# Performance work log

Measured on AMD Instinct MI355X. Metric: run time of the kernel, lower is better.

## Reference

```python
import jax, jax.numpy as jnp
import numpy as np

B, T, DSEQ = 4096, 128, 128
DMEAN, DPRIOR = 256, 256
H, DOUT = 256, 128
NEXP, SCALE = 4, 0.1
NUM_EDGES = max(1, int(B * B * 0.05))  # static top-k size


def setup_inputs() -> dict:
    key = jax.random.key(0)
    ks = jax.random.split(key, 20)
    def n(k, shape):
        return jax.random.normal(k, shape, dtype=jnp.float32) * 0.02
    z = lambda *s: jnp.zeros(s, jnp.float32)
    return {
        "input_seq": jax.random.normal(ks[0], (B, T, DSEQ), dtype=jnp.float32),
        "mean_embedding": jax.random.normal(ks[1], (B, DMEAN), dtype=jnp.float32),
        "prior_target": jax.random.normal(ks[2], (B, DPRIOR), dtype=jnp.float32),
        "gru_Wih0": n(ks[3], (3 * H, DSEQ)), "gru_Whh0": n(ks[4], (3 * H, H)),
        "gru_bih0": z(3 * H), "gru_bhh0": z(3 * H),
        "gru_Wih1": n(ks[5], (3 * H, H)), "gru_Whh1": n(ks[6], (3 * H, H)),
        "gru_bih1": z(3 * H), "gru_bhh1": z(3 * H),
        "fc_mean_W": n(ks[7], (H, DMEAN)), "fc_mean_b": z(H),
        "gru_fc_W": n(ks[8], (DOUT, 2 * H)), "gru_fc_b": z(DOUT),
        "gcn1_W": n(ks[9], (H, DPRIOR)), "gcn1_b": z(H),
        "gcn2_W": n(ks[10], (H, H)), "gcn2_b": z(H),
        "prior_fc_W": n(ks[11], (DOUT, H)), "prior_fc_b": z(DOUT),
        "expert_W": n(ks[12], (NEXP, DOUT, DOUT)),
        "attn1_W": n(ks[13], (DOUT, 2 * DOUT)), "attn1_b": z(DOUT),
        "attn2_W": n(ks[14], (NEXP, DOUT)), "attn2_b": z(NEXP),
    }


def _gru_layer(x, Wih, Whh, bih, bhh):
    # x: [B,T,D]; PyTorch GRU cell equations
    h_dim = Whh.shape[1]
    def step(h, xt):
        gi = xt @ Wih.T + bih            # [B,3H]
        gh = h @ Whh.T + bhh
        i_r, i_z, i_n = jnp.split(gi, 3, axis=-1)
        h_r, h_z, h_n = jnp.split(gh, 3, axis=-1)
        r = jax.nn.sigmoid(i_r + h_r)
        zg = jax.nn.sigmoid(i_z + h_z)
        ng = jnp.tanh(i_n + r * h_n)
        h_new = (1.0 - zg) * ng + zg * h
        return h_new, h_new
    h0 = jnp.zeros((x.shape[0], h_dim), x.dtype)
    _, ys = jax.lax.scan(step, h0, jnp.swapaxes(x, 0, 1))
    return jnp.swapaxes(ys, 0, 1)


def _gcn(x, W, b, src, dst, n_nodes):
    # PyG GCNConv: add self-loops, sym-normalized mean aggregation
    loop = jnp.arange(n_nodes)
    s = jnp.concatenate([src, loop])
    d = jnp.concatenate([dst, loop])
    deg = jax.ops.segment_sum(jnp.ones(s.shape, x.dtype), d, num_segments=n_nodes)
    dinv = jnp.where(deg > 0, jax.lax.rsqrt(deg), 0.0)
    norm = dinv[s] * dinv[d]                  # [E]
    xw = x @ W.T                              # [N,H]
    out = jax.ops.segment_sum(xw[s] * norm[:, None], d, num_segments=n_nodes)
    return out + b


def reference(input_seq, mean_embedding, prior_target,
              gru_Wih0, gru_Whh0, gru_bih0, gru_bhh0,
              gru_Wih1, gru_Whh1, gru_bih1, gru_bhh1,
              fc_mean_W, fc_mean_b, gru_fc_W, gru_fc_b,
              gcn1_W, gcn1_b, gcn2_W, gcn2_b,
              prior_fc_W, prior_fc_b, expert_W,
              attn1_W, attn1_b, attn2_W, attn2_b):
    # --- GRU branch ---
    h1 = _gru_layer(input_seq, gru_Wih0, gru_Whh0, gru_bih0, gru_bhh0)
    h2 = _gru_layer(h1, gru_Wih1, gru_Whh1, gru_bih1, gru_bhh1)
    last_hidden = h2[:, -1, :]
    mean_feat = jax.nn.relu(mean_embedding @ fc_mean_W.T + fc_mean_b)
    gru_feat = jnp.concatenate([last_hidden, mean_feat], axis=1)
    gru_out_proj = gru_feat @ gru_fc_W.T + gru_fc_b          # [B,DOUT]
    # --- dynamic graph build via similarity top-k ---
    sim = prior_target @ prior_target.T                      # [B,B]
    diag = jnp.arange(B)
    sim = sim.at[diag, diag].set(0.0)
    _, topk_idx = jax.lax.top_k(sim.reshape(-1), NUM_EDGES)
    row = topk_idx // B
    col = topk_idx % B
    src = jnp.concatenate([row, col])   # symmetrized edge list
    dst = jnp.concatenate([col, row])
    # --- GCN branch ---
    ph = jax.nn.relu(_gcn(prior_target, gcn1_W, gcn1_b, src, dst, B))
    ph = jax.nn.relu(_gcn(ph, gcn2_W, gcn2_b, src, dst, B))
    prior_out = ph @ prior_fc_W.T + prior_fc_b               # [B,DOUT]
    # --- attention expert gate fusion ---
    base = 0.5 * gru_out_proj + 0.5 * prior_out
    diff = gru_out_proj - prior_out
    expert_res = jnp.einsum('eod,bd->beo', expert_W, diff)   # [B,NEXP,DOUT]
    fused = jnp.concatenate([gru_out_proj, prior_out], axis=-1)
    hatt = jnp.tanh(fused @ attn1_W.T + attn1_b)
    w = jax.nn.softmax(hatt @ attn2_W.T + attn2_b, axis=-1)  # [B,NEXP]
    delta = jnp.einsum('be,beo->bo', w, expert_res)
    pred = base + SCALE * delta
    return pred, gru_out_proj, prior_out
```

## Files before the change

kernel.cpp:

```cpp
#include <hip/hip_runtime.h>
#include <hip/hip_bf16.h>

#define BB    4096
#define TT    128
#define DSEQ_ 128
#define HH    256
#define DOUT_ 128
#define NEXP_ 4
static const long NUM_EDGES_ = 838860;

typedef _Float16 f16;
typedef _Float16 f16x8 __attribute__((ext_vector_type(8)));
typedef float    f32x4 __attribute__((ext_vector_type(4)));

__global__ void pack_weights_kernel(const float* __restrict__ Wih,
                                    const float* __restrict__ Whh,
                                    f16* __restrict__ Wp, int Din)
{
    const int K = Din + HH;
    const int total = 1024 * K;
    for (int idx = blockIdx.x * 256 + threadIdx.x; idx < total; idx += gridDim.x * 256) {
        int n = idx / K, k = idx % K;
        int u = n >> 2, g = n & 3;
        float v = 0.f;
        if (k < Din) {
            if (g == 0)      v = Wih[(long)u * Din + k];
            else if (g == 1) v = Wih[(long)(256 + u) * Din + k];
            else if (g == 2) v = Wih[(long)(512 + u) * Din + k];
        } else {
            int kh = k - Din;
            if (g == 0)      v = Whh[(long)u * HH + kh];
            else if (g == 1) v = Whh[(long)(256 + u) * HH + kh];
            else if (g == 3) v = Whh[(long)(512 + u) * HH + kh];
        }
        Wp[idx] = (f16)v;
    }
}

__global__ void pack_bias_kernel(const float* __restrict__ bih,
                                 const float* __restrict__ bhh,
                                 float* __restrict__ bias)
{
    int n = blockIdx.x * 256 + threadIdx.x;
    if (n >= 1024) return;
    int u = n >> 2, g = n & 3;
    float v;
    if (g == 0)      v = bih[u] + bhh[u];
    else if (g == 1) v = bih[256 + u] + bhh[256 + u];
    else if (g == 2) v = bih[512 + u];
    else             v = bhh[512 + u];
    bias[n] = v;
}

__global__ __launch_bounds__(256) void gru_superstep(
    const f16* __restrict__ Wp0, const float* __restrict__ bias0,
    const float* __restrict__ xseq,
    const f16* __restrict__ h1_in, f16* __restrict__ h1_out, int t0,
    const f16* __restrict__ Wp1, const float* __restrict__ bias1,
    const f16* __restrict__ h1_x,
    const f16* __restrict__ h2_in, f16* __restrict__ h2_out, int t1)
{
    const int layer = blockIdx.z;
    if (layer == 0 && t0 >= TT) return;
    if (layer == 1 && t1 < 0) return;

    const f16* Wp; const float* bias;
    const f16* ax16 = nullptr;
    const f16* hprev; f16* hout;
    int xc, K; long xstride = 0, xoff = 0;
    if (layer == 0) {
        Wp = Wp0; bias = bias0; xc = DSEQ_; K = DSEQ_ + HH;
        xstride = (long)TT * DSEQ_; xoff = (long)t0 * DSEQ_;
        hprev = h1_in; hout = h1_out;
    } else {
        Wp = Wp1; bias = bias1; ax16 = h1_x; xc = HH; K = HH + HH;
        hprev = h2_in; hout = h2_out;
    }

    __shared__ f16 As[128 * 32];
    __shared__ f16 Bs[128 * 32];

    const int tid  = threadIdx.x;
    const int srow = tid >> 1;
    const int sc0  = (tid & 1) * 16;
    const long m0  = (long)blockIdx.x * 128;
    const int  n0  = blockIdx.y * 128;

    const int wave = tid >> 6, lane = tid & 63;
    const int wm = wave >> 1, wn = wave & 1;
    const int quad = lane >> 4, l15 = lane & 15;

    f32x4 acc[4][4];
#pragma unroll
    for (int i = 0; i < 4; i++)
#pragma unroll
        for (int j = 0; j < 4; j++) acc[i][j] = (f32x4){0.f, 0.f, 0.f, 0.f};

    const int nchunks = K >> 5;
    for (int kc = 0; kc < nchunks; kc++) {
        const int k0 = kc << 5;
        __syncthreads();
        {
            int kg = k0 + sc0;
            f16* dst = &As[srow * 32 + sc0];
            if (kg < xc) {
                if (layer == 0) {
                    const float* p = xseq + (m0 + srow) * xstride + xoff + kg;
#pragma unroll
                    for (int j = 0; j < 16; j += 4) {
                        float4 v = *(const float4*)(p + j);
                        dst[j] = (f16)v.x; dst[j + 1] = (f16)v.y;
                        dst[j + 2] = (f16)v.z; dst[j + 3] = (f16)v.w;
                    }
                } else {
                    const f16* p = ax16 + (m0 + srow) * HH + kg;
                    *(float4*)dst       = *(const float4*)p;
                    *(float4*)(dst + 8) = *(const float4*)(p + 8);
                }
            } else {
                const f16* p = hprev + (m0 + srow) * HH + (kg - xc);
                *(float4*)dst       = *(const float4*)p;
                *(float4*)(dst + 8) = *(const float4*)(p + 8);
            }
        }
        {
            const f16* p = Wp + (long)(n0 + srow) * K + k0 + sc0;
            f16* dst = &Bs[srow * 32 + sc0];
            *(float4*)dst       = *(const float4*)p;
            *(float4*)(dst + 8) = *(const float4*)(p + 8);
        }
        __syncthreads();

        f16x8 af[4], bf[4];
#pragma unroll
        for (int i = 0; i < 4; i++)
            af[i] = *(const f16x8*)&As[(wm * 64 + i * 16 + l15) * 32 + quad * 8];
#pragma unroll
        for (int i = 0; i < 4; i++)
            bf[i] = *(const f16x8*)&Bs[(wn * 64 + i * 16 + l15) * 32 + quad * 8];
#pragma unroll
        for (int mi = 0; mi < 4; mi++)
#pragma unroll
            for (int ni = 0; ni < 4; ni++)
                acc[mi][ni] = __builtin_amdgcn_mfma_f32_16x16x32_f16(af[mi], bf[ni], acc[mi][ni], 0, 0, 0);
    }

    const long mbase = m0 + wm * 64;
    const int  nbase = n0 + wn * 64;
#pragma unroll
    for (int mi = 0; mi < 4; mi++) {
#pragma unroll
        for (int ni = 0; ni < 4; ni++) {
            const int ncol = nbase + ni * 16 + l15;
            const float bn = bias[ncol];
#pragma unroll
            for (int reg = 0; reg < 4; reg++) {
                float v = acc[mi][ni][reg] + bn;
                const int gb = lane & ~3;
                float g0 = __shfl(v, gb + 0, 64);
                float g1 = __shfl(v, gb + 1, 64);
                float g2 = __shfl(v, gb + 2, 64);
                float g3 = __shfl(v, gb + 3, 64);
                if ((lane & 3) == 0) {
                    const long mrow = mbase + mi * 16 + quad * 4 + reg;
                    const int u = ncol >> 2;
                    float hp = (float)hprev[mrow * HH + u];
                    float r = 1.f / (1.f + __expf(-g0));
                    float z = 1.f / (1.f + __expf(-g1));
                    float ng = 1.f - 2.f / (__expf(2.f * (g2 + r * g3)) + 1.f);
                    float hn = (1.f - z) * ng + z * hp;
                    hout[mrow * HH + u] = (f16)hn;
                }
            }
        }
    }
}

__global__ __launch_bounds__(256) void gemm_bt_kernel(
    const float* __restrict__ A, const float* __restrict__ Bm, float* __restrict__ C,
    int M, int N, int K, const float* __restrict__ bias,
    const float* __restrict__ rscale, int act)
{
    __shared__ float As[16][65];
    __shared__ float Bs[16][65];
    const int tid = threadIdx.x;
    const long m0 = (long)blockIdx.x * 64;
    const int  n0 = blockIdx.y * 64;
    const int ty = tid >> 4, tx = tid & 15;
    const int mA = tid >> 2, kq = (tid & 3) * 4;
    float c[4][4] = {};
    for (int k0 = 0; k0 < K; k0 += 16) {
        __syncthreads();
        float4 va = *(const float4*)&A[(m0 + mA) * K + k0 + kq];
        As[kq + 0][mA] = va.x; As[kq + 1][mA] = va.y; As[kq + 2][mA] = va.z; As[kq + 3][mA] = va.w;
        float4 vb = *(const float4*)&Bm[(long)(n0 + mA) * K + k0 + kq];
        Bs[kq + 0][mA] = vb.x; Bs[kq + 1][mA] = vb.y; Bs[kq + 2][mA] = vb.z; Bs[kq + 3][mA] = vb.w;
        __syncthreads();
#pragma unroll
        for (int k = 0; k < 16; k++) {
            float a4[4], b4[4];
#pragma unroll
            for (int j = 0; j < 4; j++) { a4[j] = As[k][ty * 4 + j]; b4[j] = Bs[k][tx * 4 + j]; }
#pragma unroll
            for (int i = 0; i < 4; i++)
#pragma unroll
                for (int j = 0; j < 4; j++) c[i][j] = fmaf(a4[i], b4[j], c[i][j]);
        }
    }
#pragma unroll
    for (int i = 0; i < 4; i++) {
        const long m = m0 + ty * 4 + i;
        const float rs = rscale ? rscale[m] : 1.f;
#pragma unroll
        for (int j = 0; j < 4; j++) {
            const int n = n0 + tx * 4 + j;
            float v = c[i][j] * rs;
            if (bias) v += bias[n];
            if (act == 1) v = fmaxf(v, 0.f);
            else if (act == 2) v = tanhf(v);
            C[m * N + n] = v;
        }
    }
}

__global__ void zero_diag_kernel(float* __restrict__ sim)
{
    int i = blockIdx.x * 256 + threadIdx.x;
    if (i < BB) sim[(long)i * BB + i] = 0.f;
}

__device__ inline unsigned keyOf(float f)
{
    unsigned u = __float_as_uint(f);
    return (u & 0x80000000u) ? ~u : (u | 0x80000000u);
}

__global__ void hist_kernel(const float* __restrict__ sim, unsigned* __restrict__ hist,
                            const unsigned* __restrict__ state, int pass)
{
    __shared__ unsigned h[4096];
    for (int i = threadIdx.x; i < 4096; i += 256) h[i] = 0;
    __syncthreads();
    unsigned pfx1 = 0, pfx2 = 0;
    if (pass == 1) pfx1 = state[0];
    if (pass == 2) pfx2 = state[2];
    const long ntot = (long)BB * BB;
    for (long i = (long)blockIdx.x * 256 + threadIdx.x; i < ntot; i += (long)gridDim.x * 256) {
        unsigned key = keyOf(sim[i]);
        if (pass == 0) atomicAdd(&h[key >> 20], 1u);
        else if (pass == 1) { if ((key >> 20) == pfx1) atomicAdd(&h[(key >> 8) & 0xFFFu], 1u); }
        else               { if ((key >> 8) == pfx2)  atomicAdd(&h[key & 0xFFu], 1u); }
    }
    __syncthreads();
    const int nb = (pass == 2) ? 256 : 4096;
    for (int i = threadIdx.x; i < nb; i += 256)
        if (h[i]) atomicAdd(&hist[i], h[i]);
}

__global__ void scan_hist_kernel(const unsigned* __restrict__ hist, unsigned* __restrict__ state, int pass)
{
    if (threadIdx.x != 0 || blockIdx.x != 0) return;
    long k = (pass == 0) ? NUM_EDGES_ : (long)state[2 * pass - 1];
    const int nb = (pass == 2) ? 256 : 4096;
    long cum = 0; int b = nb - 1;
    for (; b >= 0; b--) { cum += hist[b]; if (cum >= k) break; }
    long kk = k - (cum - hist[b]);
    if (pass == 0) { state[0] = (unsigned)b; state[1] = (unsigned)kk; }
    else if (pass == 1) { state[2] = (state[0] << 12) | (unsigned)b; state[3] = (unsigned)kk; }
    else {
        unsigned key = (state[2] << 8) | (unsigned)b;
        state[4] = key;
        unsigned u = (key & 0x80000000u) ? (key ^ 0x80000000u) : ~key;
        state[5] = u;
    }
}

__global__ void degree_kernel(const float* __restrict__ sim, const unsigned* __restrict__ state,
                              float* __restrict__ dinv)
{
    const float thr = __uint_as_float(state[5]);
    const int d = blockIdx.x;
    const float* row = sim + (long)d * BB;
    int cnt = 0;
    for (int s = threadIdx.x; s < BB; s += 256) cnt += (row[s] >= thr) ? 1 : 0;
    for (int o = 32; o; o >>= 1) cnt += __shfl_down(cnt, o, 64);
    __shared__ int sh[4];
    if ((threadIdx.x & 63) == 0) sh[threadIdx.x >> 6] = cnt;
    __syncthreads();
    if (threadIdx.x == 0) {
        int tot = sh[0] + sh[1] + sh[2] + sh[3];
        dinv[d] = rsqrtf((float)(2 * tot + 1));
    }
}

__global__ __launch_bounds__(256) void gcn_agg_kernel(
    const float* __restrict__ sim, const float* __restrict__ xws,
    const float* __restrict__ dinv, const float* __restrict__ bias,
    const unsigned* __restrict__ state, float* __restrict__ out)
{
    const float thr = __uint_as_float(state[5]);
    __shared__ float As[16][65];
    __shared__ float Bs[16][65];
    const int tid = threadIdx.x;
    const long m0 = (long)blockIdx.x * 64;
    const int  n0 = blockIdx.y * 64;
    const int ty = tid >> 4, tx = tid & 15;
    const int mA = tid >> 2, kq = (tid & 3) * 4;
    const int kB = tid >> 4, nq = (tid & 15) * 4;
    float c[4][4] = {};
    for (int s0 = 0; s0 < BB; s0 += 16) {
        __syncthreads();
        float4 va = *(const float4*)&sim[(m0 + mA) * (long)BB + s0 + kq];
        As[kq + 0][mA] = (va.x >= thr) ? 1.f : 0.f;
        As[kq + 1][mA] = (va.y >= thr) ? 1.f : 0.f;
        As[kq + 2][mA] = (va.z >= thr) ? 1.f : 0.f;
        As[kq + 3][mA] = (va.w >= thr) ? 1.f : 0.f;
        float4 vb = *(const float4*)&xws[(long)(s0 + kB) * HH + n0 + nq];
        Bs[kB][nq + 0] = vb.x; Bs[kB][nq + 1] = vb.y; Bs[kB][nq + 2] = vb.z; Bs[kB][nq + 3] = vb.w;
        __syncthreads();
#pragma unroll
        for (int k = 0; k < 16; k++) {
            float a4[4], b4[4];
#pragma unroll
            for (int j = 0; j < 4; j++) { a4[j] = As[k][ty * 4 + j]; b4[j] = Bs[k][tx * 4 + j]; }
#pragma unroll
            for (int i = 0; i < 4; i++)
#pragma unroll
                for (int j = 0; j < 4; j++) c[i][j] = fmaf(a4[i], b4[j], c[i][j]);
        }
    }
#pragma unroll
    for (int i = 0; i < 4; i++) {
        const long m = m0 + ty * 4 + i;
        const float dv = dinv[m];
#pragma unroll
        for (int j = 0; j < 4; j++) {
            const int n = n0 + tx * 4 + j;
            float v = dv * (2.f * c[i][j] + xws[m * HH + n]) + bias[n];
            out[m * HH + n] = fmaxf(v, 0.f);
        }
    }
}

__global__ void build_gru_feat_kernel(const f16* __restrict__ h2, const float* __restrict__ mf,
                                      float* __restrict__ gf)
{
    long i = (long)blockIdx.x * 256 + threadIdx.x;
    if (i >= (long)BB * 512) return;
    long b = i >> 9; int c = (int)(i & 511);
    gf[i] = (c < 256) ? (float)h2[b * HH + c] : mf[b * HH + (c - 256)];
}

__global__ void build_fused_diff_kernel(const float* __restrict__ g, const float* __restrict__ p,
                                        float* __restrict__ fused, float* __restrict__ diff)
{
    long i = (long)blockIdx.x * 256 + threadIdx.x;
    if (i >= (long)BB * 256) return;
    long b = i >> 8; int c = (int)(i & 255);
    if (c < 128) {
        float gv = g[b * 128 + c], pv = p[b * 128 + c];
        fused[i] = gv;
        diff[b * 128 + c] = gv - pv;
    } else {
        fused[i] = p[b * 128 + (c - 128)];
    }
}

__global__ __launch_bounds__(128) void final_kernel(
    const float* __restrict__ hatt, const float* __restrict__ attn2W, const float* __restrict__ attn2b,
    const float* __restrict__ er, const float* __restrict__ g, const float* __restrict__ p,
    float* __restrict__ pred)
{
    const int b = blockIdx.x;
    __shared__ float w4[4];
    __shared__ float hrow[128];
    const int tid = threadIdx.x;
    hrow[tid] = hatt[(long)b * 128 + tid];
    __syncthreads();
    if (tid < 4) {
        float s = attn2b[tid];
        for (int d = 0; d < 128; d++) s += hrow[d] * attn2W[tid * 128 + d];
        w4[tid] = s;
    }
    __syncthreads();
    if (tid == 0) {
        float mx = fmaxf(fmaxf(w4[0], w4[1]), fmaxf(w4[2], w4[3]));
        float e0 = __expf(w4[0] - mx), e1 = __expf(w4[1] - mx);
        float e2 = __expf(w4[2] - mx), e3 = __expf(w4[3] - mx);
        float inv = 1.f / (e0 + e1 + e2 + e3);
        w4[0] = e0 * inv; w4[1] = e1 * inv; w4[2] = e2 * inv; w4[3] = e3 * inv;
    }
    __syncthreads();
    const long off = (long)b * 128 + tid;
    const long E = (long)BB * DOUT_;
    float base = 0.5f * g[off] + 0.5f * p[off];
    float delta = w4[0] * er[off] + w4[1] * er[off + E] + w4[2] * er[off + 2 * E] + w4[3] * er[off + 3 * E];
    pred[off] = base + 0.1f * delta;
}

extern "C" void kernel_launch(void* const* d_in, const int* in_sizes, int n_in,
                              void* d_out, int out_size, void* d_ws, size_t ws_size,
                              hipStream_t stream)
{
    const float* input_seq  = (const float*)d_in[0];
    const float* mean_emb   = (const float*)d_in[1];
    const float* prior      = (const float*)d_in[2];
    const float* Wih0       = (const float*)d_in[3];
    const float* Whh0       = (const float*)d_in[4];
    const float* bih0       = (const float*)d_in[5];
    const float* bhh0       = (const float*)d_in[6];
    const float* Wih1       = (const float*)d_in[7];
    const float* Whh1       = (const float*)d_in[8];
    const float* bih1       = (const float*)d_in[9];
    const float* bhh1       = (const float*)d_in[10];
    const float* fc_mean_W  = (const float*)d_in[11];
    const float* fc_mean_b  = (const float*)d_in[12];
    const float* gru_fc_W   = (const float*)d_in[13];
    const float* gru_fc_b   = (const float*)d_in[14];
    const float* gcn1_W     = (const float*)d_in[15];
    const float* gcn1_b     = (const float*)d_in[16];
    const float* gcn2_W     = (const float*)d_in[17];
    const float* gcn2_b     = (const float*)d_in[18];
    const float* prior_fc_W = (const float*)d_in[19];
    const float* prior_fc_b = (const float*)d_in[20];
    const float* expert_W   = (const float*)d_in[21];
    const float* attn1_W    = (const float*)d_in[22];
    const float* attn1_b    = (const float*)d_in[23];
    const float* attn2_W    = (const float*)d_in[24];
    const float* attn2_b    = (const float*)d_in[25];

    float* out_pred = (float*)d_out;
    float* out_g    = out_pred + (long)BB * DOUT_;
    float* out_p    = out_g + (long)BB * DOUT_;

    char* base = (char*)d_ws;
    size_t off = 0;
    auto alloc = [&](size_t bytes) -> char* {
        char* p = base + off;
        off = (off + bytes + 255) & ~(size_t)255;
        return p;
    };
    f16*   wp0    = (f16*)alloc((size_t)1024 * 384 * 2);
    f16*   wp1    = (f16*)alloc((size_t)1024 * 512 * 2);
    float* bias0  = (float*)alloc(1024 * 4);
    float* bias1  = (float*)alloc(1024 * 4);
    f16*   h1b[2]; h1b[0] = (f16*)alloc((size_t)BB * HH * 2); h1b[1] = (f16*)alloc((size_t)BB * HH * 2);
    f16*   h2b[2]; h2b[0] = (f16*)alloc((size_t)BB * HH * 2); h2b[1] = (f16*)alloc((size_t)BB * HH * 2);
    float* sim    = (float*)alloc((size_t)BB * BB * 4);
    unsigned* hist  = (unsigned*)alloc(4096 * 4);
    unsigned* state = (unsigned*)alloc(256);
    float* dinv   = (float*)alloc(BB * 4);
    float* mf     = (float*)alloc((size_t)BB * HH * 4);
    float* gf     = (float*)alloc((size_t)BB * 2 * HH * 4);
    float* xws1   = (float*)alloc((size_t)BB * HH * 4);
    float* ph1    = (float*)alloc((size_t)BB * HH * 4);
    float* xws2   = (float*)alloc((size_t)BB * HH * 4);
    float* ph2    = (float*)alloc((size_t)BB * HH * 4);
    float* diffb  = (float*)alloc((size_t)BB * DOUT_ * 4);
    float* fusedb = (float*)alloc((size_t)BB * 2 * DOUT_ * 4);
    float* hatt   = (float*)alloc((size_t)BB * DOUT_ * 4);
    float* er     = (float*)alloc((size_t)NEXP_ * BB * DOUT_ * 4);
    if (off > ws_size) return;

    pack_weights_kernel<<<1536, 256, 0, stream>>>(Wih0, Whh0, wp0, DSEQ_);
    pack_weights_kernel<<<2048, 256, 0, stream>>>(Wih1, Whh1, wp1, HH);
    pack_bias_kernel<<<4, 256, 0, stream>>>(bih0, bhh0, bias0);
    pack_bias_kernel<<<4, 256, 0, stream>>>(bih1, bhh1, bias1);
    hipMemsetAsync(h1b[0], 0, (size_t)BB * HH * 2, stream);
    hipMemsetAsync(h1b[1], 0, (size_t)BB * HH * 2, stream);
    hipMemsetAsync(h2b[0], 0, (size_t)BB * HH * 2, stream);
    hipMemsetAsync(h2b[1], 0, (size_t)BB * HH * 2, stream);

    for (int tau = 0; tau <= TT; tau++) {
        gru_superstep<<<dim3(32, 8, 2), 256, 0, stream>>>(
            wp0, bias0, input_seq, h1b[tau & 1], h1b[(tau + 1) & 1], tau,
            wp1, bias1, h1b[tau & 1], h2b[tau & 1], h2b[(tau + 1) & 1], tau - 1);
    }
    const f16* h2fin = h2b[(TT + 1) & 1];

    gemm_bt_kernel<<<dim3(64, 4), 256, 0, stream>>>(mean_emb, fc_mean_W, mf, BB, HH, 256, fc_mean_b, nullptr, 1);
    build_gru_feat_kernel<<<(BB * 512) / 256, 256, 0, stream>>>(h2fin, mf, gf);
    gemm_bt_kernel<<<dim3(64, 2), 256, 0, stream>>>(gf, gru_fc_W, out_g, BB, DOUT_, 512, gru_fc_b, nullptr, 0);

    gemm_bt_kernel<<<dim3(64, 64), 256, 0, stream>>>(prior, prior, sim, BB, BB, 256, nullptr, nullptr, 0);
    zero_diag_kernel<<<16, 256, 0, stream>>>(sim);
    for (int pass = 0; pass < 3; pass++) {
        hipMemsetAsync(hist, 0, 4096 * 4, stream);
        hist_kernel<<<1024, 256, 0, stream>>>(sim, hist, state, pass);
        scan_hist_kernel<<<1, 64, 0, stream>>>(hist, state, pass);
    }
    degree_kernel<<<BB, 256, 0, stream>>>(sim, state, dinv);

    gemm_bt_kernel<<<dim3(64, 4), 256, 0, stream>>>(prior, gcn1_W, xws1, BB, HH, 256, nullptr, dinv, 0);
    gcn_agg_kernel<<<dim3(64, 4), 256, 0, stream>>>(sim, xws1, dinv, gcn1_b, state, ph1);
    gemm_bt_kernel<<<dim3(64, 4), 256, 0, stream>>>(ph1, gcn2_W, xws2, BB, HH, 256, nullptr, dinv, 0);
    gcn_agg_kernel<<<dim3(64, 4), 256, 0, stream>>>(sim, xws2, dinv, gcn2_b, state, ph2);
    gemm_bt_kernel<<<dim3(64, 2), 256, 0, stream>>>(ph2, prior_fc_W, out_p, BB, DOUT_, 256, prior_fc_b, nullptr, 0);

    build_fused_diff_kernel<<<(BB * 256) / 256, 256, 0, stream>>>(out_g, out_p, fusedb, diffb);
    for (int e = 0; e < NEXP_; e++)
        gemm_bt_kernel<<<dim3(64, 2), 256, 0, stream>>>(diffb, expert_W + (long)e * DOUT_ * DOUT_,
                                                        er + (long)e * BB * DOUT_, BB, DOUT_, DOUT_,
                                                        nullptr, nullptr, 0);
    gemm_bt_kernel<<<dim3(64, 2), 256, 0, stream>>>(fusedb, attn1_W, hatt, BB, DOUT_, 256, attn1_b, nullptr, 2);
    final_kernel<<<BB, 128, 0, stream>>>(hatt, attn2_W, attn2_b, er, out_g, out_p, out_pred);
}
```

Baseline: 6.207 ms.

## Move similarity and GCN aggregation GEMMs to fp16 MFMA with async LDS loads

The GRU superstep now loads its operands through global_load_lds direct-to-LDS transfers via a shared mm_async helper. The similarity matrix is computed with MFMA using a split hi/lo fp16 packing (three products) to keep near-fp32 accuracy, and the diagonal is zeroed inside the same kernel. The two GCN aggregation GEMMs over the 4096x4096 thresholded adjacency now run on fp16 MFMA with a split-K of four, then a combine kernel reduces the partials. Workspace buffers are aliased into one shared region to save memory. The fp16 rounding of the aggregated features and the hi/lo approximation of the similarity could change top-k tie-breaking and accuracy.

```diff
diff --git a/kernel.cpp b/kernel.cpp
--- a/kernel.cpp
+++ b/kernel.cpp
@@ -12,6 +12,10 @@
 typedef _Float16 f16;
 typedef _Float16 f16x8 __attribute__((ext_vector_type(8)));
 typedef float    f32x4 __attribute__((ext_vector_type(4)));
+
+#define GLL(gp, lp) __builtin_amdgcn_global_load_lds( \
+    (const __attribute__((address_space(1))) void*)(gp), \
+    (__attribute__((address_space(3))) void*)(lp), 16, 0, 0)
 
 __global__ void pack_weights_kernel(const float* __restrict__ Wih,
                                     const float* __restrict__ Whh,
@@ -52,6 +56,41 @@
     bias[n] = v;
 }
 
+__device__ __forceinline__ void mm_async(
+    f32x4 (&acc)[4][4], f16* __restrict__ As, f16* __restrict__ Bs,
+    const f16* __restrict__ Ag, long lda, const f16* __restrict__ Bg, long ldb,
+    int kChunks, int wave, int lane)
+{
+    const int r0 = wave * 32 + (lane >> 2);
+    const int ce = (lane & 3) * 8;
+    const int wm = wave >> 1, wn = wave & 1;
+    const int quad = lane >> 4, l15 = lane & 15;
+    const f16* ag0 = Ag + (long)r0 * lda + ce;
+    const f16* ag1 = ag0 + 16 * lda;
+    const f16* bg0 = Bg + (long)r0 * ldb + ce;
+    const f16* bg1 = bg0 + 16 * ldb;
+    f16* asw = As + wave * 1024;
+    f16* bsw = Bs + wave * 1024;
+    for (int kc = 0; kc < kChunks; kc++) {
+        __syncthreads();
+        GLL(ag0, asw); GLL(ag1, asw + 512);
+        GLL(bg0, bsw); GLL(bg1, bsw + 512);
+        ag0 += 32; ag1 += 32; bg0 += 32; bg1 += 32;
+        __syncthreads();
+        f16x8 af[4], bf[4];
+#pragma unroll
+        for (int i = 0; i < 4; i++) {
+            af[i] = *(const f16x8*)&As[(wm * 64 + i * 16 + l15) * 32 + quad * 8];
+            bf[i] = *(const f16x8*)&Bs[(wn * 64 + i * 16 + l15) * 32 + quad * 8];
+        }
+#pragma unroll
+        for (int mi = 0; mi < 4; mi++)
+#pragma unroll
+            for (int ni = 0; ni < 4; ni++)
+                acc[mi][ni] = __builtin_amdgcn_mfma_f32_16x16x32_f16(af[mi], bf[ni], acc[mi][ni], 0, 0, 0);
+    }
+}
+
 __global__ __launch_bounds__(256) void gru_superstep(
     const f16* __restrict__ Wp0, const float* __restrict__ bias0,
     const float* __restrict__ xseq,
@@ -64,31 +103,14 @@
     if (layer == 0 && t0 >= TT) return;
     if (layer == 1 && t1 < 0) return;
 
-    const f16* Wp; const float* bias;
-    const f16* ax16 = nullptr;
-    const f16* hprev; f16* hout;
-    int xc, K; long xstride = 0, xoff = 0;
-    if (layer == 0) {
-        Wp = Wp0; bias = bias0; xc = DSEQ_; K = DSEQ_ + HH;
-        xstride = (long)TT * DSEQ_; xoff = (long)t0 * DSEQ_;
-        hprev = h1_in; hout = h1_out;
-    } else {
-        Wp = Wp1; bias = bias1; ax16 = h1_x; xc = HH; K = HH + HH;
-        hprev = h2_in; hout = h2_out;
-    }
-
-    __shared__ f16 As[128 * 32];
-    __shared__ f16 Bs[128 * 32];
-
-    const int tid  = threadIdx.x;
-    const int srow = tid >> 1;
-    const int sc0  = (tid & 1) * 16;
-    const long m0  = (long)blockIdx.x * 128;
-    const int  n0  = blockIdx.y * 128;
-
+    __shared__ f16 As[4096];
+    __shared__ f16 Bs[4096];
+    const int tid = threadIdx.x;
     const int wave = tid >> 6, lane = tid & 63;
     const int wm = wave >> 1, wn = wave & 1;
     const int quad = lane >> 4, l15 = lane & 15;
+    const long m0 = (long)blockIdx.x * 128;
+    const int  n0 = blockIdx.y * 128;
 
     f32x4 acc[4][4];
 #pragma unroll
@@ -96,53 +118,50 @@
 #pragma unroll
         for (int j = 0; j < 4; j++) acc[i][j] = (f32x4){0.f, 0.f, 0.f, 0.f};
 
-    const int nchunks = K >> 5;
-    for (int kc = 0; kc < nchunks; kc++) {
-        const int k0 = kc << 5;
-        __syncthreads();
-        {
-            int kg = k0 + sc0;
-            f16* dst = &As[srow * 32 + sc0];
-            if (kg < xc) {
-                if (layer == 0) {
-                    const float* p = xseq + (m0 + srow) * xstride + xoff + kg;
-#pragma unroll
-                    for (int j = 0; j < 16; j += 4) {
-                        float4 v = *(const float4*)(p + j);
-                        dst[j] = (f16)v.x; dst[j + 1] = (f16)v.y;
-                        dst[j + 2] = (f16)v.z; dst[j + 3] = (f16)v.w;
-                    }
-                } else {
-                    const f16* p = ax16 + (m0 + srow) * HH + kg;
-                    *(float4*)dst       = *(const float4*)p;
-                    *(float4*)(dst + 8) = *(const float4*)(p + 8);
-                }
-            } else {
-                const f16* p = hprev + (m0 + srow) * HH + (kg - xc);
-                *(float4*)dst       = *(const float4*)p;
-                *(float4*)(dst + 8) = *(const float4*)(p + 8);
+    const f16* hprev; f16* hout; const float* bias;
+    if (layer == 0) {
+        hprev = h1_in; hout = h1_out; bias = bias0;
+        const int arow = tid >> 1, ac0 = (tid & 1) * 16;
+        const float* ap = xseq + (m0 + arow) * ((long)TT * DSEQ_) + (long)t0 * DSEQ_ + ac0;
+        const int r0 = wave * 32 + (lane >> 2);
+        const int ce = (lane & 3) * 8;
+        const f16* bg0 = Wp0 + (long)(n0 + r0) * 384 + ce;
+        const f16* bg1 = bg0 + 16 * 384;
+        f16* bsw = Bs + wave * 1024;
+        for (int kc = 0; kc < 4; kc++) {
+            float4 v0 = *(const float4*)(ap + 0);
+            float4 v1 = *(const float4*)(ap + 4);
+            float4 v2 = *(const float4*)(ap + 8);
+            float4 v3 = *(const float4*)(ap + 12);
+            ap += 32;
+            __syncthreads();
+            f16x8 w0, w1;
+            w0[0] = (f16)v0.x; w0[1] = (f16)v0.y; w0[2] = (f16)v0.z; w0[3] = (f16)v0.w;
+            w0[4] = (f16)v1.x; w0[5] = (f16)v1.y; w0[6] = (f16)v1.z; w0[7] = (f16)v1.w;
+            w1[0] = (f16)v2.x; w1[1] = (f16)v2.y; w1[2] = (f16)v2.z; w1[3] = (f16)v2.w;
+            w1[4] = (f16)v3.x; w1[5] = (f16)v3.y; w1[6] = (f16)v3.z; w1[7] = (f16)v3.w;
+            *(f16x8*)&As[arow * 32 + ac0]     = w0;
+            *(f16x8*)&As[arow * 32 + ac0 + 8] = w1;
+            GLL(bg0, bsw); GLL(bg1, bsw + 512);
+            bg0 += 32; bg1 += 32;
+            __syncthreads();
+            f16x8 af[4], bf[4];
+#pragma unroll
+            for (int i = 0; i < 4; i++) {
+                af[i] = *(const f16x8*)&As[(wm * 64 + i * 16 + l15) * 32 + quad * 8];
+                bf[i] = *(const f16x8*)&Bs[(wn * 64 + i * 16 + l15) * 32 + quad * 8];
             }
+#pragma unroll
+            for (int mi = 0; mi < 4; mi++)
+#pragma unroll
+                for (int ni = 0; ni < 4; ni++)
+                    acc[mi][ni] = __builtin_amdgcn_mfma_f32_16x16x32_f16(af[mi], bf[ni], acc[mi][ni], 0, 0, 0);
         }
-        {
-            const f16* p = Wp + (long)(n0 + srow) * K + k0 + sc0;
-            f16* dst = &Bs[srow * 32 + sc0];
-            *(float4*)dst       = *(const float4*)p;
-            *(float4*)(dst + 8) = *(const float4*)(p + 8);
-        }
-        __syncthreads();
-
-        f16x8 af[4], bf[4];
-#pragma unroll
-        for (int i = 0; i < 4; i++)
-            af[i] = *(const f16x8*)&As[(wm * 64 + i * 16 + l15) * 32 + quad * 8];
-#pragma unroll
-        for (int i = 0; i < 4; i++)
-            bf[i] = *(const f16x8*)&Bs[(wn * 64 + i * 16 + l15) * 32 + quad * 8];
-#pragma unroll
-        for (int mi = 0; mi < 4; mi++)
-#pragma unroll
-            for (int ni = 0; ni < 4; ni++)
-                acc[mi][ni] = __builtin_amdgcn_mfma_f32_16x16x32_f16(af[mi], bf[ni], acc[mi][ni], 0, 0, 0);
+        mm_async(acc, As, Bs, h1_in + m0 * HH, HH, Wp0 + (long)n0 * 384 + 128, 384, 8, wave, lane);
+    } else {
+        hprev = h2_in; hout = h2_out; bias = bias1;
+        mm_async(acc, As, Bs, h1_x + m0 * HH, HH, Wp1 + (long)n0 * 512, 512, 8, wave, lane);
+        mm_async(acc, As, Bs, h2_in + m0 * HH, HH, Wp1 + (long)n0 * 512 + 256, 512, 8, wave, lane);
     }
 
     const long mbase = m0 + wm * 64;
@@ -176,6 +195,217 @@
     }
 }
 
+__global__ void sim_pack_kernel(const float* __restrict__ prior,
+                                f16* __restrict__ pA, f16* __restrict__ pB)
+{
+    int i = blockIdx.x * 256 + threadIdx.x;
+    if (i >= BB * 256) return;
+    int b = i >> 8, k = i & 255;
+    float v = prior[i];
+    f16 hi = (f16)v;
+    f16 lo = (f16)(v - (float)hi);
+    long r = (long)b * 768;
+    pA[r + k] = hi; pA[r + 256 + k] = hi; pA[r + 512 + k] = lo;
+    pB[r + k] = hi; pB[r + 256 + k] = lo; pB[r + 512 + k] = hi;
+}
+
+__global__ __launch_bounds__(256) void sim_mm_kernel(
+    const f16* __restrict__ pA, const f16* __restrict__ pB, float* __restrict__ sim)
+{
+    __shared__ f16 As[4096];
+    __shared__ f16 Bs[4096];
+    const int tid = threadIdx.x;
+    const int wave = tid >> 6, lane = tid & 63;
+    const int wm = wave >> 1, wn = wave & 1;
+    const int quad = lane >> 4, l15 = lane & 15;
+    const long m0 = (long)blockIdx.x * 128;
+    const int  n0 = blockIdx.y * 128;
+    f32x4 acc[4][4];
+#pragma unroll
+    for (int i = 0; i < 4; i++)
+#pragma unroll
+        for (int j = 0; j < 4; j++) acc[i][j] = (f32x4){0.f, 0.f, 0.f, 0.f};
+    mm_async(acc, As, Bs, pA + m0 * 768, 768, pB + (long)n0 * 768, 768, 24, wave, lane);
+    const long mbase = m0 + wm * 64;
+    const int  nbase = n0 + wn * 64;
+#pragma unroll
+    for (int mi = 0; mi < 4; mi++)
+#pragma unroll
+        for (int ni = 0; ni < 4; ni++)
+#pragma unroll
+            for (int reg = 0; reg < 4; reg++) {
+                long row = mbase + mi * 16 + quad * 4 + reg;
+                int col = nbase + ni * 16 + l15;
+                float v = acc[mi][ni][reg];
+                if (row == (long)col) v = 0.f;
+                sim[row * BB + col] = v;
+            }
+}
+
+__device__ inline unsigned keyOf(float f)
+{
+    unsigned u = __float_as_uint(f);
+    return (u & 0x80000000u) ? ~u : (u | 0x80000000u);
+}
+
+__global__ void hist_kernel(const float* __restrict__ sim, unsigned* __restrict__ hist,
+                            const unsigned* __restrict__ state, int pass)
+{
+    __shared__ unsigned h[4096];
+    for (int i = threadIdx.x; i < 4096; i += 256) h[i] = 0;
+    __syncthreads();
+    unsigned pfx1 = 0, pfx2 = 0;
+    if (pass == 1) pfx1 = state[0];
+    if (pass == 2) pfx2 = state[2];
+    const long ntot = (long)BB * BB;
+    for (long i = (long)blockIdx.x * 256 + threadIdx.x; i < ntot; i += (long)gridDim.x * 256) {
+        unsigned key = keyOf(sim[i]);
+        if (pass == 0) atomicAdd(&h[key >> 20], 1u);
+        else if (pass == 1) { if ((key >> 20) == pfx1) atomicAdd(&h[(key >> 8) & 0xFFFu], 1u); }
+        else               { if ((key >> 8) == pfx2)  atomicAdd(&h[key & 0xFFu], 1u); }
+    }
+    __syncthreads();
+    const int nb = (pass == 2) ? 256 : 4096;
+    for (int i = threadIdx.x; i < nb; i += 256)
+        if (h[i]) atomicAdd(&hist[i], h[i]);
+}
+
+__global__ void scan_hist_kernel(const unsigned* __restrict__ hist,
+                                 unsigned* __restrict__ state, int pass)
+{
+    __shared__ unsigned hl[4096];
+    const int nb = (pass == 2) ? 256 : 4096;
+    for (int i = threadIdx.x; i < nb; i += 256) hl[i] = hist[i];
+    __syncthreads();
+    if (threadIdx.x != 0 || blockIdx.x != 0) return;
+    long k = (pass == 0) ? NUM_EDGES_ : (long)state[2 * pass - 1];
+    long cum = 0; int b = nb - 1;
+    for (; b >= 0; b--) { cum += hl[b]; if (cum >= k) break; }
+    long kk = k - (cum - hl[b]);
+    if (pass == 0) { state[0] = (unsigned)b; state[1] = (unsigned)kk; }
+    else if (pass == 1) { state[2] = (state[0] << 12) | (unsigned)b; state[3] = (unsigned)kk; }
+    else {
+        unsigned key = (state[2] << 8) | (unsigned)b;
+        state[4] = key;
+        unsigned u = (key & 0x80000000u) ? (key ^ 0x80000000u) : ~key;
+        state[5] = u;
+    }
+}
+
+__global__ void degree_kernel(const float* __restrict__ sim, const unsigned* __restrict__ state,
+                              float* __restrict__ dinv)
+{
+    const float thr = __uint_as_float(state[5]);
+    const int d = blockIdx.x;
+    const float* row = sim + (long)d * BB;
+    int cnt = 0;
+    for (int s = threadIdx.x; s < BB; s += 256) cnt += (row[s] >= thr) ? 1 : 0;
+    for (int o = 32; o; o >>= 1) cnt += __shfl_down(cnt, o, 64);
+    __shared__ int sh[4];
+    if ((threadIdx.x & 63) == 0) sh[threadIdx.x >> 6] = cnt;
+    __syncthreads();
+    if (threadIdx.x == 0) {
+        int tot = sh[0] + sh[1] + sh[2] + sh[3];
+        dinv[d] = rsqrtf((float)(2 * tot + 1));
+    }
+}
+
+__global__ void txp_kernel(const float* __restrict__ xws, f16* __restrict__ bT)
+{
+    int i = blockIdx.x * 256 + threadIdx.x;
+    if (i >= BB * 256) return;
+    int n = i >> 12, m = i & 4095;
+    bT[(long)n * BB + m] = (f16)xws[(long)m * 256 + n];
+}
+
+__global__ __launch_bounds__(256) void gcn_mm_kernel(
+    const float* __restrict__ sim, const f16* __restrict__ bT,
+    const unsigned* __restrict__ state, float* __restrict__ ps)
+{
+    const float thr = __uint_as_float(state[5]);
+    __shared__ f16 As[4096];
+    __shared__ f16 Bs[4096];
+    const int tid = threadIdx.x;
+    const int wave = tid >> 6, lane = tid & 63;
+    const int wm = wave >> 1, wn = wave & 1;
+    const int quad = lane >> 4, l15 = lane & 15;
+    const long m0 = (long)blockIdx.x * 128;
+    const int  n0 = blockIdx.y * 128;
+    const long kbase = (long)blockIdx.z * 1024;
+    f32x4 acc[4][4];
+#pragma unroll
+    for (int i = 0; i < 4; i++)
+#pragma unroll
+        for (int j = 0; j < 4; j++) acc[i][j] = (f32x4){0.f, 0.f, 0.f, 0.f};
+
+    const int arow = tid >> 1, ac0 = (tid & 1) * 16;
+    const float* ap = sim + (m0 + arow) * (long)BB + kbase + ac0;
+    const int r0 = wave * 32 + (lane >> 2);
+    const int ce = (lane & 3) * 8;
+    const f16* bg0 = bT + (long)(n0 + r0) * BB + kbase + ce;
+    const f16* bg1 = bg0 + 16 * BB;
+    f16* bsw = Bs + wave * 1024;
+    const f16 one = (f16)1.f, zero = (f16)0.f;
+    for (int kc = 0; kc < 32; kc++) {
+        float4 v0 = *(const float4*)(ap + 0);
+        float4 v1 = *(const float4*)(ap + 4);
+        float4 v2 = *(const float4*)(ap + 8);
+        float4 v3 = *(const float4*)(ap + 12);
+        ap += 32;
+        __syncthreads();
+        f16x8 w0, w1;
+        w0[0] = v0.x >= thr ? one : zero; w0[1] = v0.y >= thr ? one : zero;
+        w0[2] = v0.z >= thr ? one : zero; w0[3] = v0.w >= thr ? one : zero;
+        w0[4] = v1.x >= thr ? one : zero; w0[5] = v1.y >= thr ? one : zero;
+        w0[6] = v1.z >= thr ? one : zero; w0[7] = v1.w >= thr ? one : zero;
+        w1[0] = v2.x >= thr ? one : zero; w1[1] = v2.y >= thr ? one : zero;
+        w1[2] = v2.z >= thr ? one : zero; w1[3] = v2.w >= thr ? one : zero;
+        w1[4] = v3.x >= thr ? one : zero; w1[5] = v3.y >= thr ? one : zero;
+        w1[6] = v3.z >= thr ? one : zero; w1[7] = v3.w >= thr ? one : zero;
+        *(f16x8*)&As[arow * 32 + ac0]     = w0;
+        *(f16x8*)&As[arow * 32 + ac0 + 8] = w1;
+        GLL(bg0, bsw); GLL(bg1, bsw + 512);
+        bg0 += 32; bg1 += 32;
+        __syncthreads();
+        f16x8 af[4], bf[4];
+#pragma unroll
+        for (int i = 0; i < 4; i++) {
+            af[i] = *(const f16x8*)&As[(wm * 64 + i * 16 + l15) * 32 + quad * 8];
+            bf[i] = *(const f16x8*)&Bs[(wn * 64 + i * 16 + l15) * 32 + quad * 8];
+        }
+#pragma unroll
+        for (int mi = 0; mi < 4; mi++)
+#pragma unroll
+            for (int ni = 0; ni < 4; ni++)
+                acc[mi][ni] = __builtin_amdgcn_mfma_f32_16x16x32_f16(af[mi], bf[ni], acc[mi][ni], 0, 0, 0);
+    }
+    const long mbase = m0 + wm * 64;
+    const int  nbase = n0 + wn * 64;
+    float* pbase = ps + (long)blockIdx.z * BB * 256;
+#pragma unroll
+    for (int mi = 0; mi < 4; mi++)
+#pragma unroll
+        for (int ni = 0; ni < 4; ni++)
+#pragma unroll
+            for (int reg = 0; reg < 4; reg++) {
+                long row = mbase + mi * 16 + quad * 4 + reg;
+                int col = nbase + ni * 16 + l15;
+                pbase[row * 256 + col] = acc[mi][ni][reg];
+            }
+}
+
+__global__ void gcn_combine_kernel(const float* __restrict__ ps, const float* __restrict__ xws,
+                                   const float* __restrict__ dinv, const float* __restrict__ b,
+                                   float* __restrict__ out)
+{
+    const long S = (long)BB * 256;
+    long i = (long)blockIdx.x * 256 + threadIdx.x;
+    if (i >= S) return;
+    float s = ps[i] + ps[i + S] + ps[i + 2 * S] + ps[i + 3 * S];
+    long m = i >> 8; int n = (int)(i & 255);
+    out[i] = fmaxf(dinv[m] * (2.f * s + xws[i]) + b[n], 0.f);
+}
+
 __global__ __launch_bounds__(256) void gemm_bt_kernel(
     const float* __restrict__ A, const float* __restrict__ Bm, float* __restrict__ C,
     int M, int N, int K, const float* __restrict__ bias,
@@ -219,125 +449,6 @@
             if (act == 1) v = fmaxf(v, 0.f);
             else if (act == 2) v = tanhf(v);
             C[m * N + n] = v;
-        }
-    }
-}
-
-__global__ void zero_diag_kernel(float* __restrict__ sim)
-{
-    int i = blockIdx.x * 256 + threadIdx.x;
-    if (i < BB) sim[(long)i * BB + i] = 0.f;
-}
-
-__device__ inline unsigned keyOf(float f)
-{
-    unsigned u = __float_as_uint(f);
-    return (u & 0x80000000u) ? ~u : (u | 0x80000000u);
-}
-
-__global__ void hist_kernel(const float* __restrict__ sim, unsigned* __restrict__ hist,
-                            const unsigned* __restrict__ state, int pass)
-{
-    __shared__ unsigned h[4096];
-    for (int i = threadIdx.x; i < 4096; i += 256) h[i] = 0;
-    __syncthreads();
-    unsigned pfx1 = 0, pfx2 = 0;
-    if (pass == 1) pfx1 = state[0];
-    if (pass == 2) pfx2 = state[2];
-    const long ntot = (long)BB * BB;
-    for (long i = (long)blockIdx.x * 256 + threadIdx.x; i < ntot; i += (long)gridDim.x * 256) {
-        unsigned key = keyOf(sim[i]);
-        if (pass == 0) atomicAdd(&h[key >> 20], 1u);
-        else if (pass == 1) { if ((key >> 20) == pfx1) atomicAdd(&h[(key >> 8) & 0xFFFu], 1u); }
-        else               { if ((key >> 8) == pfx2)  atomicAdd(&h[key & 0xFFu], 1u); }
-    }
-    __syncthreads();
-    const int nb = (pass == 2) ? 256 : 4096;
-    for (int i = threadIdx.x; i < nb; i += 256)
-        if (h[i]) atomicAdd(&hist[i], h[i]);
-}
-
-__global__ void scan_hist_kernel(const unsigned* __restrict__ hist, unsigned* __restrict__ state, int pass)
-{
-    if (threadIdx.x != 0 || blockIdx.x != 0) return;
-    long k = (pass == 0) ? NUM_EDGES_ : (long)state[2 * pass - 1];
-    const int nb = (pass == 2) ? 256 : 4096;
-    long cum = 0; int b = nb - 1;
-    for (; b >= 0; b--) { cum += hist[b]; if (cum >= k) break; }
-    long kk = k - (cum - hist[b]);
-    if (pass == 0) { state[0] = (unsigned)b; state[1] = (unsigned)kk; }
-    else if (pass == 1) { state[2] = (state[0] << 12) | (unsigned)b; state[3] = (unsigned)kk; }
-    else {
-        unsigned key = (state[2] << 8) | (unsigned)b;
-        state[4] = key;
-        unsigned u = (key & 0x80000000u) ? (key ^ 0x80000000u) : ~key;
-        state[5] = u;
-    }
-}
-
-__global__ void degree_kernel(const float* __restrict__ sim, const unsigned* __restrict__ state,
-                              float* __restrict__ dinv)
-{
-    const float thr = __uint_as_float(state[5]);
-    const int d = blockIdx.x;
-    const float* row = sim + (long)d * BB;
-    int cnt = 0;
-    for (int s = threadIdx.x; s < BB; s += 256) cnt += (row[s] >= thr) ? 1 : 0;
-    for (int o = 32; o; o >>= 1) cnt += __shfl_down(cnt, o, 64);
-    __shared__ int sh[4];
-    if ((threadIdx.x & 63) == 0) sh[threadIdx.x >> 6] = cnt;
-    __syncthreads();
-    if (threadIdx.x == 0) {
-        int tot = sh[0] + sh[1] + sh[2] + sh[3];
-        dinv[d] = rsqrtf((float)(2 * tot + 1));
-    }
-}
-
-__global__ __launch_bounds__(256) void gcn_agg_kernel(
-    const float* __restrict__ sim, const float* __restrict__ xws,
-    const float* __restrict__ dinv, const float* __restrict__ bias,
-    const unsigned* __restrict__ state, float* __restrict__ out)
-{
-    const float thr = __uint_as_float(state[5]);
-    __shared__ float As[16][65];
-    __shared__ float Bs[16][65];
-    const int tid = threadIdx.x;
-    const long m0 = (long)blockIdx.x * 64;
-    const int  n0 = blockIdx.y * 64;
-    const int ty = tid >> 4, tx = tid & 15;
-    const int mA = tid >> 2, kq = (tid & 3) * 4;
-    const int kB = tid >> 4, nq = (tid & 15) * 4;
-    float c[4][4] = {};
-    for (int s0 = 0; s0 < BB; s0 += 16) {
-        __syncthreads();
-        float4 va = *(const float4*)&sim[(m0 + mA) * (long)BB + s0 + kq];
-        As[kq + 0][mA] = (va.x >= thr) ? 1.f : 0.f;
-        As[kq + 1][mA] = (va.y >= thr) ? 1.f : 0.f;
-        As[kq + 2][mA] = (va.z >= thr) ? 1.f : 0.f;
-        As[kq + 3][mA] = (va.w >= thr) ? 1.f : 0.f;
-        float4 vb = *(const float4*)&xws[(long)(s0 + kB) * HH + n0 + nq];
-        Bs[kB][nq + 0] = vb.x; Bs[kB][nq + 1] = vb.y; Bs[kB][nq + 2] = vb.z; Bs[kB][nq + 3] = vb.w;
-        __syncthreads();
-#pragma unroll
-        for (int k = 0; k < 16; k++) {
-            float a4[4], b4[4];
-#pragma unroll
-            for (int j = 0; j < 4; j++) { a4[j] = As[k][ty * 4 + j]; b4[j] = Bs[k][tx * 4 + j]; }
-#pragma unroll
-            for (int i = 0; i < 4; i++)
-#pragma unroll
-                for (int j = 0; j < 4; j++) c[i][j] = fmaf(a4[i], b4[j], c[i][j]);
-        }
-    }
-#pragma unroll
-    for (int i = 0; i < 4; i++) {
-        const long m = m0 + ty * 4 + i;
-        const float dv = dinv[m];
-#pragma unroll
-        for (int j = 0; j < 4; j++) {
-            const int n = n0 + tx * 4 + j;
-            float v = dv * (2.f * c[i][j] + xws[m * HH + n]) + bias[n];
-            out[m * HH + n] = fmaxf(v, 0.f);
         }
     }
 }
@@ -433,6 +544,7 @@
     float* out_g    = out_pred + (long)BB * DOUT_;
     float* out_p    = out_g + (long)BB * DOUT_;
 
+    const size_t MB = 1u << 20;
     char* base = (char*)d_ws;
     size_t off = 0;
     auto alloc = [&](size_t bytes) -> char* {
@@ -450,17 +562,23 @@
     unsigned* hist  = (unsigned*)alloc(4096 * 4);
     unsigned* state = (unsigned*)alloc(256);
     float* dinv   = (float*)alloc(BB * 4);
-    float* mf     = (float*)alloc((size_t)BB * HH * 4);
-    float* gf     = (float*)alloc((size_t)BB * 2 * HH * 4);
     float* xws1   = (float*)alloc((size_t)BB * HH * 4);
     float* ph1    = (float*)alloc((size_t)BB * HH * 4);
     float* xws2   = (float*)alloc((size_t)BB * HH * 4);
     float* ph2    = (float*)alloc((size_t)BB * HH * 4);
-    float* diffb  = (float*)alloc((size_t)BB * DOUT_ * 4);
-    float* fusedb = (float*)alloc((size_t)BB * 2 * DOUT_ * 4);
-    float* hatt   = (float*)alloc((size_t)BB * DOUT_ * 4);
-    float* er     = (float*)alloc((size_t)NEXP_ * BB * DOUT_ * 4);
+    f16*   xwsT16 = (f16*)alloc((size_t)256 * BB * 2);
+    char*  region = alloc(20 * MB);
     if (off > ws_size) return;
+
+    float* mf     = (float*)(region);
+    float* gf     = (float*)(region + 5 * MB);
+    f16*   packA  = (f16*)(region);
+    f16*   packB  = (f16*)(region + 7 * MB);
+    float* ps     = (float*)(region);
+    float* diffb  = (float*)(region);
+    float* fusedb = (float*)(region + 3 * MB);
+    float* hatt   = (float*)(region + 8 * MB);
+    float* er     = (float*)(region + 11 * MB);
 
     pack_weights_kernel<<<1536, 256, 0, stream>>>(Wih0, Whh0, wp0, DSEQ_);
     pack_weights_kernel<<<2048, 256, 0, stream>>>(Wih1, Whh1, wp1, HH);
@@ -482,19 +600,23 @@
     build_gru_feat_kernel<<<(BB * 512) / 256, 256, 0, stream>>>(h2fin, mf, gf);
     gemm_bt_kernel<<<dim3(64, 2), 256, 0, stream>>>(gf, gru_fc_W, out_g, BB, DOUT_, 512, gru_fc_b, nullptr, 0);
 
-    gemm_bt_kernel<<<dim3(64, 64), 256, 0, stream>>>(prior, prior, sim, BB, BB, 256, nullptr, nullptr, 0);
-    zero_diag_kernel<<<16, 256, 0, stream>>>(sim);
+    sim_pack_kernel<<<4096, 256, 0, stream>>>(prior, packA, packB);
+    sim_mm_kernel<<<dim3(32, 32), 256, 0, stream>>>(packA, packB, sim);
     for (int pass = 0; pass < 3; pass++) {
         hipMemsetAsync(hist, 0, 4096 * 4, stream);
         hist_kernel<<<1024, 256, 0, stream>>>(sim, hist, state, pass);
-        scan_hist_kernel<<<1, 64, 0, stream>>>(hist, state, pass);
+        scan_hist_kernel<<<1, 256, 0, stream>>>(hist, state, pass);
     }
     degree_kernel<<<BB, 256, 0, stream>>>(sim, state, dinv);
 
     gemm_bt_kernel<<<dim3(64, 4), 256, 0, stream>>>(prior, gcn1_W, xws1, BB, HH, 256, nullptr, dinv, 0);
-    gcn_agg_kernel<<<dim3(64, 4), 256, 0, stream>>>(sim, xws1, dinv, gcn1_b, state, ph1);
+    txp_kernel<<<4096, 256, 0, stream>>>(xws1, xwsT16);
+    gcn_mm_kernel<<<dim3(32, 2, 4), 256, 0, stream>>>(sim, xwsT16, state, ps);
+    gcn_combine_kernel<<<4096, 256, 0, stream>>>(ps, xws1, dinv, gcn1_b, ph1);
     gemm_bt_kernel<<<dim3(64, 4), 256, 0, stream>>>(ph1, gcn2_W, xws2, BB, HH, 256, nullptr, dinv, 0);
-    gcn_agg_kernel<<<dim3(64, 4), 256, 0, stream>>>(sim, xws2, dinv, gcn2_b, state, ph2);
+    txp_kernel<<<4096, 256, 0, stream>>>(xws2, xwsT16);
+    gcn_mm_kernel<<<dim3(32, 2, 4), 256, 0, stream>>>(sim, xwsT16, state, ps);
+    gcn_combine_kernel<<<4096, 256, 0, stream>>>(ps, xws2, dinv, gcn2_b, ph2);
     gemm_bt_kernel<<<dim3(64, 2), 256, 0, stream>>>(ph2, prior_fc_W, out_p, BB, DOUT_, 256, prior_fc_b, nullptr, 0);
 
     build_fused_diff_kernel<<<(BB * 256) / 256, 256, 0, stream>>>(out_g, out_p, fusedb, diffb);
```

After: 5.198 ms. 16.3% less time.
